# Optimization experiments

Hardware: AMD Instinct MI355X
Metric: run time of the kernel (lower is better)

## Reference

```python
import jax, jax.numpy as jnp
import numpy as np

B, L, E = 4096, 50, 128


def setup_inputs() -> dict:
    key = jax.random.key(0)
    ks = jax.random.split(key, 12)
    s = 1.0 / np.sqrt(E)
    return {
        "A": jax.random.uniform(ks[0], (B, L, 2 * L), dtype=jnp.float32),
        "hidden": jax.random.normal(ks[1], (B, L, E), dtype=jnp.float32),
        "w_ih": jax.random.normal(ks[2], (3 * E, 2 * E), dtype=jnp.float32) * s,
        "w_hh": jax.random.normal(ks[3], (3 * E, E), dtype=jnp.float32) * s,
        "b_ih": jax.random.normal(ks[4], (3 * E,), dtype=jnp.float32) * s,
        "b_hh": jax.random.normal(ks[5], (3 * E,), dtype=jnp.float32) * s,
        "b_iah": jax.random.normal(ks[6], (E,), dtype=jnp.float32) * s,
        "b_ioh": jax.random.normal(ks[7], (E,), dtype=jnp.float32) * s,
        "w_in": jax.random.normal(ks[8], (E, E), dtype=jnp.float32) * s,
        "b_in": jax.random.normal(ks[9], (E,), dtype=jnp.float32) * s,
        "w_out": jax.random.normal(ks[10], (E, E), dtype=jnp.float32) * s,
        "b_out": jax.random.normal(ks[11], (E,), dtype=jnp.float32) * s,
    }


STEP = 1


def _gnn_cell(A, hidden, w_ih, w_hh, b_ih, b_hh, b_iah, b_ioh, w_in, b_in, w_out, b_out):
    L_ = A.shape[1]
    # linear_edge_in / linear_edge_out (torch Linear: x @ W.T + b)
    h_in = jnp.einsum('ble,fe->blf', hidden, w_in) + b_in
    h_out = jnp.einsum('ble,fe->blf', hidden, w_out) + b_out
    # adjacency propagation: A = [A_in | A_out] along last dim
    input_in = jnp.matmul(A[:, :, :L_], h_in) + b_iah     # [B,L,E]
    input_out = jnp.matmul(A[:, :, L_:2 * L_], h_out) + b_ioh
    inputs = jnp.concatenate([input_in, input_out], axis=2)  # [B,L,2E]
    gi = jnp.einsum('blf,gf->blg', inputs, w_ih) + b_ih      # [B,L,3E]
    gh = jnp.einsum('ble,ge->blg', hidden, w_hh) + b_hh      # [B,L,3E]
    i_r, i_i, i_n = jnp.split(gi, 3, axis=2)
    h_r, h_i, h_n = jnp.split(gh, 3, axis=2)
    reset_gate = jax.nn.sigmoid(i_r + h_r)
    input_gate = jax.nn.sigmoid(i_i + h_i)
    new_gate = jnp.tanh(i_n + reset_gate * h_n)
    return (1 - input_gate) * hidden + input_gate * new_gate


def reference(A, hidden, w_ih, w_hh, b_ih, b_hh, b_iah, b_ioh, w_in, b_in, w_out, b_out):
    for _ in range(STEP):
        hidden = _gnn_cell(A, hidden, w_ih, w_hh, b_ih, b_hh, b_iah, b_ioh, w_in, b_in, w_out, b_out)
    return hidden
```

## Files before the change

kernel.cpp:

```cpp
#include <hip/hip_runtime.h>


using f32x4 = __attribute__((ext_vector_type(4))) float;
using s16x8 = __attribute__((ext_vector_type(8))) short;
using s16x4 = __attribute__((ext_vector_type(4))) short;

#define MFMA(a, b, c) __builtin_amdgcn_mfma_f32_16x16x32_bf16((a), (b), (c), 0, 0, 0)

__device__ __forceinline__ unsigned short f2bf(float x) {
    unsigned u = __float_as_uint(x);
    u += 0x7fffu + ((u >> 16) & 1u);
    return (unsigned short)(u >> 16);
}
__device__ __forceinline__ float bf2f(unsigned short b) {
    return __uint_as_float(((unsigned)b) << 16);
}

__global__ void wconv_kernel(const float* __restrict__ w_in, const float* __restrict__ w_out,
                             const float* __restrict__ w_hh, const float* __restrict__ w_ih,
                             unsigned short* __restrict__ W1, unsigned short* __restrict__ Wih) {
    int i = blockIdx.x * 256 + threadIdx.x;
    if (i < 81920) {
        float v = (i < 16384) ? w_in[i] : (i < 32768) ? w_out[i - 16384] : w_hh[i - 32768];
        W1[i] = f2bf(v);
    } else if (i < 180224) {
        int j = i - 81920;
        Wih[j] = f2bf(w_ih[j]);
    }
}

#define LDS_BYTES 143360

__launch_bounds__(512, 1)
__global__ void gnn_kernel(const float* __restrict__ A, const float* __restrict__ H,
                           const unsigned short* __restrict__ W1, const unsigned short* __restrict__ Wih,
                           const float* __restrict__ b_ih, const float* __restrict__ b_hh,
                           const float* __restrict__ b_iah, const float* __restrict__ b_ioh,
                           const float* __restrict__ b_in, const float* __restrict__ b_out,
                           float* __restrict__ out) {
    extern __shared__ char smem[];
    unsigned short* sHhi = (unsigned short*)(smem + 0);
    unsigned short* sHlo = (unsigned short*)(smem + 17408);
    unsigned short* sAhi = (unsigned short*)(smem + 34816);
    unsigned short* sAlo = (unsigned short*)(smem + 52224);
    unsigned short* sThi = (unsigned short*)(smem + 69632);
    unsigned short* sTlo = (unsigned short*)(smem + 106496);
    unsigned short* sIhi = (unsigned short*)(smem + 69632);
    unsigned short* sIlo = (unsigned short*)(smem + 103424);

    const int b    = blockIdx.x;
    const int tid  = threadIdx.x;
    const int wv   = tid >> 6;
    const int lane = tid & 63;
    const int l16  = lane & 15;
    const int l4   = lane >> 4;

    const float* Hb = H + (size_t)b * 6400;
    const float* Ab = A + (size_t)b * 5000;

    #pragma unroll
    for (int it = 0; it < 16; ++it) {
        int idx = it * 512 + tid;
        int r = idx >> 7, c = idx & 127;
        float x = (r < 50) ? Hb[r * 128 + c] : 0.f;
        unsigned short xh = f2bf(x);
        sHhi[r * 136 + c] = xh;
        sHlo[r * 136 + c] = f2bf(x - bf2f(xh));
        float a = 0.f;
        if (r < 50) {
            if (c < 64) { if (c < 50) a = Ab[r * 100 + c]; }
            else        { int k = c - 64; if (k < 50) a = Ab[r * 100 + 50 + k]; }
        }
        unsigned short ah16 = f2bf(a);
        sAhi[r * 136 + c] = ah16;
        sAlo[r * 136 + c] = f2bf(a - bf2f(ah16));
    }
    __syncthreads();

    const f32x4 vzero = {0.f, 0.f, 0.f, 0.f};

    f32x4 acc_io[2][4];
    f32x4 acc_gh[3][4];
    #pragma unroll
    for (int t = 0; t < 2; ++t)
        #pragma unroll
        for (int m = 0; m < 4; ++m) acc_io[t][m] = vzero;
    #pragma unroll
    for (int t = 0; t < 3; ++t)
        #pragma unroll
        for (int m = 0; m < 4; ++m) acc_gh[t][m] = vzero;

    #pragma unroll 1
    for (int kt = 0; kt < 4; ++kt) {
        s16x8 ah[4], al[4];
        #pragma unroll
        for (int mt = 0; mt < 4; ++mt) {
            int off = (mt * 16 + l16) * 136 + kt * 32 + l4 * 8;
            ah[mt] = *(const s16x8*)(sHhi + off);
            al[mt] = *(const s16x8*)(sHlo + off);
        }
        s16x8 bfr[5];
        #pragma unroll
        for (int t = 0; t < 5; ++t) {
            int row = (wv + 8 * t) * 16 + l16;
            bfr[t] = *(const s16x8*)(W1 + row * 128 + kt * 32 + l4 * 8);
        }
        #pragma unroll
        for (int t = 0; t < 5; ++t) {
            #pragma unroll
            for (int mt = 0; mt < 4; ++mt) {
                if (t < 2) {
                    f32x4 acc = acc_io[t][mt];
                    acc = MFMA(ah[mt], bfr[t], acc);
                    acc = MFMA(al[mt], bfr[t], acc);
                    acc_io[t][mt] = acc;
                } else {
                    f32x4 acc = acc_gh[t - 2][mt];
                    acc = MFMA(ah[mt], bfr[t], acc);
                    acc = MFMA(al[mt], bfr[t], acc);
                    acc_gh[t - 2][mt] = acc;
                }
            }
        }
    }
    #pragma unroll
    for (int t = 0; t < 2; ++t) {
        int n = (wv + 8 * t) * 16 + l16;
        float bias = (n < 128) ? b_in[n] : b_out[n - 128];
        #pragma unroll
        for (int mt = 0; mt < 4; ++mt) {
            int mb = mt * 16 + l4 * 4;
            s16x4 vhi, vlo;
            #pragma unroll
            for (int r = 0; r < 4; ++r) {
                float x = acc_io[t][mt][r] + bias;
                unsigned short xh = f2bf(x);
                vhi[r] = (short)xh;
                vlo[r] = (short)f2bf(x - bf2f(xh));
            }
            *(s16x4*)(sThi + n * 72 + mb) = vhi;
            *(s16x4*)(sTlo + n * 72 + mb) = vlo;
        }
    }
    __syncthreads();

    const int p = wv >> 2, q = wv & 3;
    f32x4 acc2[2][4];
    #pragma unroll
    for (int t = 0; t < 2; ++t)
        #pragma unroll
        for (int m = 0; m < 4; ++m) acc2[t][m] = vzero;

    #pragma unroll 1
    for (int kt = 0; kt < 2; ++kt) {
        s16x8 ah[4], al[4];
        #pragma unroll
        for (int mt = 0; mt < 4; ++mt) {
            int off = (mt * 16 + l16) * 136 + p * 64 + kt * 32 + l4 * 8;
            ah[mt] = *(const s16x8*)(sAhi + off);
            al[mt] = *(const s16x8*)(sAlo + off);
        }
        #pragma unroll
        for (int t = 0; t < 2; ++t) {
            int hr = p * 128 + (q + 4 * t) * 16 + l16;
            int boff = hr * 72 + kt * 32 + l4 * 8;
            s16x8 bh = *(const s16x8*)(sThi + boff);
            s16x8 bl = *(const s16x8*)(sTlo + boff);
            #pragma unroll
            for (int mt = 0; mt < 4; ++mt) {
                f32x4 acc = acc2[t][mt];
                acc = MFMA(ah[mt], bh, acc);
                acc = MFMA(ah[mt], bl, acc);
                acc = MFMA(al[mt], bh, acc);
                acc2[t][mt] = acc;
            }
        }
    }
    __syncthreads();
    #pragma unroll
    for (int t = 0; t < 2; ++t) {
        int n = p * 128 + (q + 4 * t) * 16 + l16;
        float bias = (n < 128) ? b_iah[n] : b_ioh[n - 128];
        #pragma unroll
        for (int mt = 0; mt < 4; ++mt) {
            int mb = mt * 16 + l4 * 4;
            #pragma unroll
            for (int r = 0; r < 4; ++r) {
                float x = acc2[t][mt][r] + bias;
                unsigned short xh = f2bf(x);
                sIhi[(mb + r) * 264 + n] = xh;
                sIlo[(mb + r) * 264 + n] = f2bf(x - bf2f(xh));
            }
        }
    }
    __syncthreads();

    f32x4 acc_n[4];
    #pragma unroll
    for (int m = 0; m < 4; ++m) acc_n[m] = vzero;

    #pragma unroll 1
    for (int kt = 0; kt < 8; ++kt) {
        s16x8 ah[4], al[4];
        #pragma unroll
        for (int mt = 0; mt < 4; ++mt) {
            int off = (mt * 16 + l16) * 264 + kt * 32 + l4 * 8;
            ah[mt] = *(const s16x8*)(sIhi + off);
            al[mt] = *(const s16x8*)(sIlo + off);
        }
        s16x8 bfr[3];
        #pragma unroll
        for (int t = 0; t < 3; ++t) {
            int row = (wv + 8 * t) * 16 + l16;
            bfr[t] = *(const s16x8*)(Wih + row * 256 + kt * 32 + l4 * 8);
        }
        #pragma unroll
        for (int t = 0; t < 3; ++t) {
            #pragma unroll
            for (int mt = 0; mt < 4; ++mt) {
                if (t < 2) {
                    f32x4 acc = acc_gh[t][mt];
                    acc = MFMA(ah[mt], bfr[t], acc);
                    acc = MFMA(al[mt], bfr[t], acc);
                    acc_gh[t][mt] = acc;
                } else {
                    f32x4 acc = acc_n[mt];
                    acc = MFMA(ah[mt], bfr[t], acc);
                    acc = MFMA(al[mt], bfr[t], acc);
                    acc_n[mt] = acc;
                }
            }
        }
    }

    {
        const int e = wv * 16 + l16;
        const float br   = b_ih[e]       + b_hh[e];
        const float bi   = b_ih[128 + e] + b_hh[128 + e];
        const float bn_i = b_ih[256 + e];
        const float bn_h = b_hh[256 + e];
        float* Ob = out + (size_t)b * 6400;
        #pragma unroll
        for (int mt = 0; mt < 4; ++mt) {
            #pragma unroll
            for (int r = 0; r < 4; ++r) {
                int m = mt * 16 + l4 * 4 + r;
                if (m < 50) {
                    float argr = acc_gh[0][mt][r] + br;
                    float argi = acc_gh[1][mt][r] + bi;
                    float i_n  = acc_n[mt][r] + bn_i;
                    float h_n  = acc_gh[2][mt][r] + bn_h;
                    float rg = 1.f / (1.f + __expf(-argr));
                    float ig = 1.f / (1.f + __expf(-argi));
                    float ta = i_n + rg * h_n;
                    ta = fminf(fmaxf(ta, -30.f), 30.f);
                    float ex = __expf(2.f * ta);
                    float ng = (ex - 1.f) / (ex + 1.f);
                    float h0 = bf2f(sHhi[m * 136 + e]) + bf2f(sHlo[m * 136 + e]);
                    Ob[m * 128 + e] = h0 + ig * (ng - h0);
                }
            }
        }
    }
}

extern "C" void kernel_launch(void* const* d_in, const int* in_sizes, int n_in,
                              void* d_out, int out_size, void* d_ws, size_t ws_size,
                              hipStream_t stream) {
    const float* A     = (const float*)d_in[0];
    const float* hidden= (const float*)d_in[1];
    const float* w_ih  = (const float*)d_in[2];
    const float* w_hh  = (const float*)d_in[3];
    const float* b_ih  = (const float*)d_in[4];
    const float* b_hh  = (const float*)d_in[5];
    const float* b_iah = (const float*)d_in[6];
    const float* b_ioh = (const float*)d_in[7];
    const float* w_in  = (const float*)d_in[8];
    const float* b_in  = (const float*)d_in[9];
    const float* w_out = (const float*)d_in[10];
    const float* b_out = (const float*)d_in[11];
    float* out = (float*)d_out;

    unsigned short* W1  = (unsigned short*)d_ws;
    unsigned short* Wih = W1 + 81920;

    wconv_kernel<<<704, 256, 0, stream>>>(w_in, w_out, w_hh, w_ih, W1, Wih);

    const int nbatch = in_sizes[1] / 6400;
    (void)hipFuncSetAttribute((const void*)gnn_kernel,
                              hipFuncAttributeMaxDynamicSharedMemorySize, LDS_BYTES);
    gnn_kernel<<<nbatch, 512, LDS_BYTES, stream>>>(A, hidden, W1, Wih,
                                                   b_ih, b_hh, b_iah, b_ioh,
                                                   b_in, b_out, out);
}
```

Before: 615.9 us.

## Vectorize staging loads, preload weight fragments, drop A low split, double-buffer LDS reads

Input staging of H and A now uses float4/float2 global loads and packed bf16 conversion (v_cvt_pk_bf16_f32), with targeted zeroing of padding. The A matrix is no longer split into hi/lo bf16 parts, which removes one LDS plane and one MFMA per product in the adjacency stage. Weight fragments for W1 and Wih are loaded into registers up front, and the LDS fragment reads in the GEMM loops are double-buffered with full unrolling so global and LDS latency can overlap with MFMA work. The cost is much higher register pressure and lower precision for A.

```diff
diff --git a/kernel.cpp b/kernel.cpp
--- a/kernel.cpp
+++ b/kernel.cpp
@@ -3,7 +3,7 @@
 
 using f32x4 = __attribute__((ext_vector_type(4))) float;
 using s16x8 = __attribute__((ext_vector_type(8))) short;
-using s16x4 = __attribute__((ext_vector_type(4))) short;
+using u32x2 = __attribute__((ext_vector_type(2))) unsigned;
 
 #define MFMA(a, b, c) __builtin_amdgcn_mfma_f32_16x16x32_bf16((a), (b), (c), 0, 0, 0)
 
@@ -14,6 +14,11 @@
 }
 __device__ __forceinline__ float bf2f(unsigned short b) {
     return __uint_as_float(((unsigned)b) << 16);
+}
+__device__ __forceinline__ unsigned pkbf(float a, float b) {
+    unsigned r;
+    asm("v_cvt_pk_bf16_f32 %0, %1, %2" : "=v"(r) : "v"(a), "v"(b));
+    return r;
 }
 
 __global__ void wconv_kernel(const float* __restrict__ w_in, const float* __restrict__ w_out,
@@ -29,7 +34,7 @@
     }
 }
 
-#define LDS_BYTES 143360
+#define LDS_BYTES 125952
 
 __launch_bounds__(512, 1)
 __global__ void gnn_kernel(const float* __restrict__ A, const float* __restrict__ H,
@@ -42,11 +47,10 @@
     unsigned short* sHhi = (unsigned short*)(smem + 0);
     unsigned short* sHlo = (unsigned short*)(smem + 17408);
     unsigned short* sAhi = (unsigned short*)(smem + 34816);
-    unsigned short* sAlo = (unsigned short*)(smem + 52224);
-    unsigned short* sThi = (unsigned short*)(smem + 69632);
-    unsigned short* sTlo = (unsigned short*)(smem + 106496);
-    unsigned short* sIhi = (unsigned short*)(smem + 69632);
-    unsigned short* sIlo = (unsigned short*)(smem + 103424);
+    unsigned short* sThi = (unsigned short*)(smem + 52224);
+    unsigned short* sTlo = (unsigned short*)(smem + 89088);
+    unsigned short* sIhi = (unsigned short*)(smem + 52224);
+    unsigned short* sIlo = (unsigned short*)(smem + 86016);
 
     const int b    = blockIdx.x;
     const int tid  = threadIdx.x;
@@ -58,22 +62,67 @@
     const float* Hb = H + (size_t)b * 6400;
     const float* Ab = A + (size_t)b * 5000;
 
-    #pragma unroll
-    for (int it = 0; it < 16; ++it) {
-        int idx = it * 512 + tid;
-        int r = idx >> 7, c = idx & 127;
-        float x = (r < 50) ? Hb[r * 128 + c] : 0.f;
-        unsigned short xh = f2bf(x);
-        sHhi[r * 136 + c] = xh;
-        sHlo[r * 136 + c] = f2bf(x - bf2f(xh));
-        float a = 0.f;
-        if (r < 50) {
-            if (c < 64) { if (c < 50) a = Ab[r * 100 + c]; }
-            else        { int k = c - 64; if (k < 50) a = Ab[r * 100 + 50 + k]; }
-        }
-        unsigned short ah16 = f2bf(a);
-        sAhi[r * 136 + c] = ah16;
-        sAlo[r * 136 + c] = f2bf(a - bf2f(ah16));
+    s16x8 w1f[4][5];
+    #pragma unroll
+    for (int kt = 0; kt < 4; ++kt)
+        #pragma unroll
+        for (int t = 0; t < 5; ++t)
+            w1f[kt][t] = *(const s16x8*)(W1 + ((wv + 8 * t) * 16 + l16) * 128 + kt * 32 + l4 * 8);
+
+    {
+        const float4* H4 = (const float4*)Hb;
+        #pragma unroll
+        for (int i = 0; i < 4; ++i) {
+            int idx = i * 512 + tid;
+            if (idx < 1600) {
+                int r = idx >> 5, c = (idx & 31) * 4;
+                float4 v = H4[idx];
+                unsigned h01 = pkbf(v.x, v.y), h23 = pkbf(v.z, v.w);
+                float g0 = __uint_as_float(h01 << 16), g1 = __uint_as_float(h01 & 0xffff0000u);
+                float g2 = __uint_as_float(h23 << 16), g3 = __uint_as_float(h23 & 0xffff0000u);
+                unsigned l01 = pkbf(v.x - g0, v.y - g1), l23 = pkbf(v.z - g2, v.w - g3);
+                u32x2 vh; vh[0] = h01; vh[1] = h23;
+                u32x2 vl; vl[0] = l01; vl[1] = l23;
+                *(u32x2*)(sHhi + r * 136 + c) = vh;
+                *(u32x2*)(sHlo + r * 136 + c) = vl;
+            }
+        }
+        #pragma unroll
+        for (int i = 0; i < 4; ++i) {
+            int idx = i * 512 + tid;
+            if (idx < 1792) {
+                int pl = idx >= 896 ? 1 : 0;
+                int j = idx - pl * 896;
+                int r = 50 + (j >> 6), c = (j & 63) * 2;
+                *(unsigned*)((pl ? sHlo : sHhi) + r * 136 + c) = 0u;
+            }
+        }
+        const float2* A2 = (const float2*)Ab;
+        #pragma unroll
+        for (int i = 0; i < 5; ++i) {
+            int idx = i * 512 + tid;
+            if (idx < 2500) {
+                int r = idx / 50, j = idx - r * 50;
+                float2 v = A2[idx];
+                int dc = (j < 25) ? (2 * j) : (2 * j + 14);
+                *(unsigned*)(sAhi + r * 136 + dc) = pkbf(v.x, v.y);
+            }
+        }
+        #pragma unroll
+        for (int i = 0; i < 4; ++i) {
+            int idx = i * 512 + tid;
+            if (idx < 1596) {
+                int r, c;
+                if (idx < 700) {
+                    r = idx / 14; int k = idx - r * 14;
+                    c = (k < 7) ? (50 + 2 * k) : (100 + 2 * k);
+                } else {
+                    int j = idx - 700;
+                    r = 50 + (j >> 6); c = (j & 63) * 2;
+                }
+                *(unsigned*)(sAhi + r * 136 + c) = 0u;
+            }
+        }
     }
     __syncthreads();
 
@@ -90,39 +139,49 @@
         #pragma unroll
         for (int m = 0; m < 4; ++m) acc_gh[t][m] = vzero;
 
-    #pragma unroll 1
+    s16x8 ah[2][4], al[2][4];
+    #pragma unroll
+    for (int mt = 0; mt < 4; ++mt) {
+        int off = (mt * 16 + l16) * 136 + l4 * 8;
+        ah[0][mt] = *(const s16x8*)(sHhi + off);
+        al[0][mt] = *(const s16x8*)(sHlo + off);
+    }
+    #pragma unroll
     for (int kt = 0; kt < 4; ++kt) {
-        s16x8 ah[4], al[4];
-        #pragma unroll
-        for (int mt = 0; mt < 4; ++mt) {
-            int off = (mt * 16 + l16) * 136 + kt * 32 + l4 * 8;
-            ah[mt] = *(const s16x8*)(sHhi + off);
-            al[mt] = *(const s16x8*)(sHlo + off);
-        }
-        s16x8 bfr[5];
-        #pragma unroll
-        for (int t = 0; t < 5; ++t) {
-            int row = (wv + 8 * t) * 16 + l16;
-            bfr[t] = *(const s16x8*)(W1 + row * 128 + kt * 32 + l4 * 8);
-        }
-        #pragma unroll
-        for (int t = 0; t < 5; ++t) {
+        const int cur = kt & 1, nxt = cur ^ 1;
+        if (kt < 3) {
+            #pragma unroll
+            for (int mt = 0; mt < 4; ++mt) {
+                int off = (mt * 16 + l16) * 136 + (kt + 1) * 32 + l4 * 8;
+                ah[nxt][mt] = *(const s16x8*)(sHhi + off);
+                al[nxt][mt] = *(const s16x8*)(sHlo + off);
+            }
+        }
+        #pragma unroll
+        for (int t = 0; t < 5; ++t)
             #pragma unroll
             for (int mt = 0; mt < 4; ++mt) {
                 if (t < 2) {
-                    f32x4 acc = acc_io[t][mt];
-                    acc = MFMA(ah[mt], bfr[t], acc);
-                    acc = MFMA(al[mt], bfr[t], acc);
-                    acc_io[t][mt] = acc;
+                    f32x4 a = acc_io[t][mt];
+                    a = MFMA(ah[cur][mt], w1f[kt][t], a);
+                    a = MFMA(al[cur][mt], w1f[kt][t], a);
+                    acc_io[t][mt] = a;
                 } else {
-                    f32x4 acc = acc_gh[t - 2][mt];
-                    acc = MFMA(ah[mt], bfr[t], acc);
-                    acc = MFMA(al[mt], bfr[t], acc);
-                    acc_gh[t - 2][mt] = acc;
-                }
-            }
-        }
-    }
+                    f32x4 a = acc_gh[t - 2][mt];
+                    a = MFMA(ah[cur][mt], w1f[kt][t], a);
+                    a = MFMA(al[cur][mt], w1f[kt][t], a);
+                    acc_gh[t - 2][mt] = a;
+                }
+            }
+    }
+
+    s16x8 wihf[8][3];
+    #pragma unroll
+    for (int kt = 0; kt < 8; ++kt)
+        #pragma unroll
+        for (int t = 0; t < 3; ++t)
+            wihf[kt][t] = *(const s16x8*)(Wih + ((wv + 8 * t) * 16 + l16) * 256 + kt * 32 + l4 * 8);
+
     #pragma unroll
     for (int t = 0; t < 2; ++t) {
         int n = (wv + 8 * t) * 16 + l16;
@@ -130,16 +189,16 @@
         #pragma unroll
         for (int mt = 0; mt < 4; ++mt) {
             int mb = mt * 16 + l4 * 4;
-            s16x4 vhi, vlo;
-            #pragma unroll
-            for (int r = 0; r < 4; ++r) {
-                float x = acc_io[t][mt][r] + bias;
-                unsigned short xh = f2bf(x);
-                vhi[r] = (short)xh;
-                vlo[r] = (short)f2bf(x - bf2f(xh));
-            }
-            *(s16x4*)(sThi + n * 72 + mb) = vhi;
-            *(s16x4*)(sTlo + n * 72 + mb) = vlo;
+            float x0 = acc_io[t][mt][0] + bias, x1 = acc_io[t][mt][1] + bias;
+            float x2 = acc_io[t][mt][2] + bias, x3 = acc_io[t][mt][3] + bias;
+            unsigned h01 = pkbf(x0, x1), h23 = pkbf(x2, x3);
+            float g0 = __uint_as_float(h01 << 16), g1 = __uint_as_float(h01 & 0xffff0000u);
+            float g2 = __uint_as_float(h23 << 16), g3 = __uint_as_float(h23 & 0xffff0000u);
+            unsigned l01 = pkbf(x0 - g0, x1 - g1), l23 = pkbf(x2 - g2, x3 - g3);
+            u32x2 vh; vh[0] = h01; vh[1] = h23;
+            u32x2 vl; vl[0] = l01; vl[1] = l23;
+            *(u32x2*)(sThi + n * 72 + mb) = vh;
+            *(u32x2*)(sTlo + n * 72 + mb) = vl;
         }
     }
     __syncthreads();
@@ -151,30 +210,31 @@
         #pragma unroll
         for (int m = 0; m < 4; ++m) acc2[t][m] = vzero;
 
-    #pragma unroll 1
-    for (int kt = 0; kt < 2; ++kt) {
-        s16x8 ah[4], al[4];
-        #pragma unroll
-        for (int mt = 0; mt < 4; ++mt) {
-            int off = (mt * 16 + l16) * 136 + p * 64 + kt * 32 + l4 * 8;
-            ah[mt] = *(const s16x8*)(sAhi + off);
-            al[mt] = *(const s16x8*)(sAlo + off);
-        }
-        #pragma unroll
-        for (int t = 0; t < 2; ++t) {
-            int hr = p * 128 + (q + 4 * t) * 16 + l16;
-            int boff = hr * 72 + kt * 32 + l4 * 8;
-            s16x8 bh = *(const s16x8*)(sThi + boff);
-            s16x8 bl = *(const s16x8*)(sTlo + boff);
-            #pragma unroll
-            for (int mt = 0; mt < 4; ++mt) {
-                f32x4 acc = acc2[t][mt];
-                acc = MFMA(ah[mt], bh, acc);
-                acc = MFMA(ah[mt], bl, acc);
-                acc = MFMA(al[mt], bh, acc);
-                acc2[t][mt] = acc;
-            }
-        }
+    {
+        s16x8 a2[2][4], th2[2][2], tl2[2][2];
+        #pragma unroll
+        for (int kt = 0; kt < 2; ++kt) {
+            #pragma unroll
+            for (int mt = 0; mt < 4; ++mt)
+                a2[kt][mt] = *(const s16x8*)(sAhi + (mt * 16 + l16) * 136 + p * 64 + kt * 32 + l4 * 8);
+            #pragma unroll
+            for (int t = 0; t < 2; ++t) {
+                int hr = p * 128 + (q + 4 * t) * 16 + l16;
+                th2[kt][t] = *(const s16x8*)(sThi + hr * 72 + kt * 32 + l4 * 8);
+                tl2[kt][t] = *(const s16x8*)(sTlo + hr * 72 + kt * 32 + l4 * 8);
+            }
+        }
+        #pragma unroll
+        for (int kt = 0; kt < 2; ++kt)
+            #pragma unroll
+            for (int t = 0; t < 2; ++t)
+                #pragma unroll
+                for (int mt = 0; mt < 4; ++mt) {
+                    f32x4 a = acc2[t][mt];
+                    a = MFMA(a2[kt][mt], th2[kt][t], a);
+                    a = MFMA(a2[kt][mt], tl2[kt][t], a);
+                    acc2[t][mt] = a;
+                }
     }
     __syncthreads();
     #pragma unroll
@@ -185,11 +245,15 @@
         for (int mt = 0; mt < 4; ++mt) {
             int mb = mt * 16 + l4 * 4;
             #pragma unroll
-            for (int r = 0; r < 4; ++r) {
-                float x = acc2[t][mt][r] + bias;
-                unsigned short xh = f2bf(x);
-                sIhi[(mb + r) * 264 + n] = xh;
-                sIlo[(mb + r) * 264 + n] = f2bf(x - bf2f(xh));
+            for (int rr = 0; rr < 4; rr += 2) {
+                float x0 = acc2[t][mt][rr] + bias, x1 = acc2[t][mt][rr + 1] + bias;
+                unsigned h = pkbf(x0, x1);
+                float g0 = __uint_as_float(h << 16), g1 = __uint_as_float(h & 0xffff0000u);
+                unsigned l = pkbf(x0 - g0, x1 - g1);
+                sIhi[(mb + rr) * 264 + n]     = (unsigned short)(h & 0xffffu);
+                sIhi[(mb + rr + 1) * 264 + n] = (unsigned short)(h >> 16);
+                sIlo[(mb + rr) * 264 + n]     = (unsigned short)(l & 0xffffu);
+                sIlo[(mb + rr + 1) * 264 + n] = (unsigned short)(l >> 16);
             }
         }
     }
@@ -199,38 +263,39 @@
     #pragma unroll
     for (int m = 0; m < 4; ++m) acc_n[m] = vzero;
 
-    #pragma unroll 1
+    #pragma unroll
+    for (int mt = 0; mt < 4; ++mt) {
+        int off = (mt * 16 + l16) * 264 + l4 * 8;
+        ah[0][mt] = *(const s16x8*)(sIhi + off);
+        al[0][mt] = *(const s16x8*)(sIlo + off);
+    }
+    #pragma unroll
     for (int kt = 0; kt < 8; ++kt) {
-        s16x8 ah[4], al[4];
-        #pragma unroll
-        for (int mt = 0; mt < 4; ++mt) {
-            int off = (mt * 16 + l16) * 264 + kt * 32 + l4 * 8;
-            ah[mt] = *(const s16x8*)(sIhi + off);
-            al[mt] = *(const s16x8*)(sIlo + off);
-        }
-        s16x8 bfr[3];
-        #pragma unroll
-        for (int t = 0; t < 3; ++t) {
-            int row = (wv + 8 * t) * 16 + l16;
-            bfr[t] = *(const s16x8*)(Wih + row * 256 + kt * 32 + l4 * 8);
-        }
-        #pragma unroll
-        for (int t = 0; t < 3; ++t) {
+        const int cur = kt & 1, nxt = cur ^ 1;
+        if (kt < 7) {
+            #pragma unroll
+            for (int mt = 0; mt < 4; ++mt) {
+                int off = (mt * 16 + l16) * 264 + (kt + 1) * 32 + l4 * 8;
+                ah[nxt][mt] = *(const s16x8*)(sIhi + off);
+                al[nxt][mt] = *(const s16x8*)(sIlo + off);
+            }
+        }
+        #pragma unroll
+        for (int t = 0; t < 3; ++t)
             #pragma unroll
             for (int mt = 0; mt < 4; ++mt) {
                 if (t < 2) {
-                    f32x4 acc = acc_gh[t][mt];
-                    acc = MFMA(ah[mt], bfr[t], acc);
-                    acc = MFMA(al[mt], bfr[t], acc);
-                    acc_gh[t][mt] = acc;
+                    f32x4 a = acc_gh[t][mt];
+                    a = MFMA(ah[cur][mt], wihf[kt][t], a);
+                    a = MFMA(al[cur][mt], wihf[kt][t], a);
+                    acc_gh[t][mt] = a;
                 } else {
-                    f32x4 acc = acc_n[mt];
-                    acc = MFMA(ah[mt], bfr[t], acc);
-                    acc = MFMA(al[mt], bfr[t], acc);
-                    acc_n[mt] = acc;
-                }
-            }
-        }
+                    f32x4 a = acc_n[mt];
+                    a = MFMA(ah[cur][mt], wihf[kt][t], a);
+                    a = MFMA(al[cur][mt], wihf[kt][t], a);
+                    acc_n[mt] = a;
+                }
+            }
     }
 
     {
```

Result: faster. 542.4 us (-11.9%).
